# Performance work log

Measured on AMD Instinct MI355X. Metric: run time of the kernel, lower is better.

Reference implementation:

```python
import jax, jax.numpy as jnp
import numpy as np

T, BS, N, D_IN, D_OUT, H_FFN = 256, 64, 128, 64, 16, 64


def setup_inputs() -> dict:
    key = jax.random.key(0)
    ks = jax.random.split(key, 12)
    s = 1.0 / float(np.sqrt(D_IN))
    uni = lambda k, shp: jax.random.uniform(k, shp, jnp.float32, -s, s)
    return {
        "u": jax.random.normal(ks[0], (T, BS, D_IN), jnp.float32),
        "y": jax.random.normal(ks[1], (T, BS, D_OUT), jnp.float32),
        "W_ih": uni(ks[2], (D_IN, D_IN)),
        "W_hh": uni(ks[3], (D_IN, D_IN)),
        "b_ih": uni(ks[4], (D_IN,)),
        "b_hh": uni(ks[5], (D_IN,)),
        "W1": uni(ks[6], (D_IN, H_FFN)),
        "b1": uni(ks[7], (H_FFN,)),
        "W2": uni(ks[8], (H_FFN, D_OUT)),
        "b2": uni(ks[9], (D_OUT,)),
        # sigma matrices are diag(abs(rand(dim))) in torch; keep the diagonal vector
        "sigma_x_diag": jax.random.uniform(ks[10], (D_IN,), jnp.float32, 0.05, 1.0),
        "sigma_y_diag": jax.random.uniform(ks[11], (D_OUT,), jnp.float32, 0.05, 1.0),
    }


def reference(u, y, W_ih, W_hh, b_ih, b_hh, W1, b1, W2, b2, sigma_x_diag, sigma_y_diag):
    bs = u.shape[1]
    base = jax.random.key(42)
    # x0 = torch.randn(bs, N, input_size)
    x0 = jax.random.normal(jax.random.fold_in(base, 2**20), (bs, N, D_IN), jnp.float32)
    # MVN .sample() is detached from sigma params in torch
    std_x = jax.lax.stop_gradient(jnp.sqrt(sigma_x_diag))
    std_y = jax.lax.stop_gradient(jnp.sqrt(sigma_y_diag))
    sig_y = jax.lax.stop_gradient(sigma_y_diag)
    LOG2PI = jnp.log(jnp.asarray(2.0 * np.pi, jnp.float32))

    def ffn(x):
        return jax.nn.relu(x @ W1 + b1) @ W2 + b2

    def step(x, inp):
        u_k, y_k, t = inp
        k = jax.random.fold_in(base, t)
        k1, k2, k3 = jax.random.split(k, 3)
        # RNNCell(tanh); u_k broadcast over the particle dim (repeat_interleave in torch)
        x = jnp.tanh(u_k[:, None, :] @ W_ih + b_ih + x @ W_hh + b_hh)  # [bs,N,D_IN]
        x = x + std_x * jax.random.normal(k1, x.shape, x.dtype)        # eta noise
        x = jax.lax.stop_gradient(x)                                    # fisher: x.detach()
        y_hat = ffn(x) + std_y * jax.random.normal(k2, (bs, N, D_OUT), x.dtype)  # eps noise
        # log N(y_hat; y_k, diag(sigma_y)), fully detached (torch uses .detach())
        d = jax.lax.stop_gradient(y_hat) - y_k[:, None, :]
        logw = (-0.5 * jnp.sum(d * d / sig_y, axis=-1)
                - 0.5 * jnp.sum(jnp.log(sig_y)) - 0.5 * D_OUT * LOG2PI)  # [bs,N]
        # softmax + multinomial(w, N, replacement=True) == categorical on logits
        I = jax.random.categorical(k3, logw, axis=-1, shape=(N, bs)).T   # [bs,N]
        x = jnp.take_along_axis(x, I[:, :, None], axis=1)                # resample
        return x, y_hat

    ts = jnp.arange(u.shape[0], dtype=jnp.int32)
    _, preds = jax.lax.scan(step, x0, (u, y, ts))
    return preds  # [T, bs, N, D_OUT]
```

## Files before the change

### kernel.cpp

```cpp
#include <hip/hip_runtime.h>
#include <stdint.h>

#define TB 512

__device__ __forceinline__ uint32_t rotl32(uint32_t v, int s) {
    return (v << s) | (v >> (32 - s));
}

__device__ __forceinline__ void threefry2x32(uint32_t k0, uint32_t k1,
                                             uint32_t c0, uint32_t c1,
                                             uint32_t& o0, uint32_t& o1) {
    const uint32_t ks2 = k0 ^ k1 ^ 0x1BD11BDAu;
    uint32_t x0 = c0 + k0;
    uint32_t x1 = c1 + k1;
    x0 += x1; x1 = rotl32(x1, 13); x1 ^= x0;
    x0 += x1; x1 = rotl32(x1, 15); x1 ^= x0;
    x0 += x1; x1 = rotl32(x1, 26); x1 ^= x0;
    x0 += x1; x1 = rotl32(x1, 6);  x1 ^= x0;
    x0 += k1;  x1 += ks2 + 1u;
    x0 += x1; x1 = rotl32(x1, 17); x1 ^= x0;
    x0 += x1; x1 = rotl32(x1, 29); x1 ^= x0;
    x0 += x1; x1 = rotl32(x1, 16); x1 ^= x0;
    x0 += x1; x1 = rotl32(x1, 24); x1 ^= x0;
    x0 += ks2; x1 += k0 + 2u;
    x0 += x1; x1 = rotl32(x1, 13); x1 ^= x0;
    x0 += x1; x1 = rotl32(x1, 15); x1 ^= x0;
    x0 += x1; x1 = rotl32(x1, 26); x1 ^= x0;
    x0 += x1; x1 = rotl32(x1, 6);  x1 ^= x0;
    x0 += k0;  x1 += k1 + 3u;
    x0 += x1; x1 = rotl32(x1, 17); x1 ^= x0;
    x0 += x1; x1 = rotl32(x1, 29); x1 ^= x0;
    x0 += x1; x1 = rotl32(x1, 16); x1 ^= x0;
    x0 += x1; x1 = rotl32(x1, 24); x1 ^= x0;
    x0 += k1;  x1 += ks2 + 4u;
    x0 += x1; x1 = rotl32(x1, 13); x1 ^= x0;
    x0 += x1; x1 = rotl32(x1, 15); x1 ^= x0;
    x0 += x1; x1 = rotl32(x1, 26); x1 ^= x0;
    x0 += x1; x1 = rotl32(x1, 6);  x1 ^= x0;
    x0 += ks2; x1 += k0 + 5u;
    o0 = x0; o1 = x1;
}

__device__ __forceinline__ uint32_t jax_random_bits(uint32_t k0, uint32_t k1, uint32_t i) {
    uint32_t o0, o1;
    threefry2x32(k0, k1, 0u, i, o0, o1);
    return o0 ^ o1;
}

__device__ __forceinline__ float erfinv_f32(float x) {
    float w = -log1pf(-x * x);
    float p;
    if (w < 5.0f) {
        w = w - 2.5f;
        p = 2.81022636e-08f;
        p = fmaf(p, w, 3.43273939e-07f);
        p = fmaf(p, w, -3.5233877e-06f);
        p = fmaf(p, w, -4.39150654e-06f);
        p = fmaf(p, w, 0.00021858087f);
        p = fmaf(p, w, -0.00125372503f);
        p = fmaf(p, w, -0.00417768164f);
        p = fmaf(p, w, 0.246640727f);
        p = fmaf(p, w, 1.50140941f);
    } else {
        w = sqrtf(w) - 3.0f;
        p = -0.000200214257f;
        p = fmaf(p, w, 0.000100950558f);
        p = fmaf(p, w, 0.00134934322f);
        p = fmaf(p, w, -0.00367342844f);
        p = fmaf(p, w, 0.00573950773f);
        p = fmaf(p, w, -0.0076224613f);
        p = fmaf(p, w, 0.00943887047f);
        p = fmaf(p, w, 1.00167406f);
        p = fmaf(p, w, 2.83297682f);
    }
    return p * x;
}

__device__ __forceinline__ float normal_from_bits(uint32_t bits) {
    float f = __uint_as_float((bits >> 9) | 0x3F800000u) - 1.0f;
    float uu = fmaxf(-0.99999994f, fmaf(f, 2.0f, -0.99999994f));
    return 1.41421354f * erfinv_f32(uu);
}

__device__ __forceinline__ float gumbel_from_bits(uint32_t bits) {
    float f = __uint_as_float((bits >> 9) | 0x3F800000u) - 1.0f;
    float uu = fmaxf(1.17549435e-38f, f + 1.17549435e-38f);
    return -logf(-logf(uu));
}

__device__ __forceinline__ float jax_normal_elem(uint32_t k0, uint32_t k1, uint32_t i) {
    return normal_from_bits(jax_random_bits(k0, k1, i));
}

__device__ __forceinline__ void step_keys(int t, uint32_t& kx0, uint32_t& kx1,
                                          uint32_t& ky0, uint32_t& ky1,
                                          uint32_t& kc0, uint32_t& kc1) {
    uint32_t kk0, kk1;
    threefry2x32(0u, 42u, 0u, (uint32_t)t, kk0, kk1);
    threefry2x32(kk0, kk1, 0u, 0u, kx0, kx1);
    threefry2x32(kk0, kk1, 0u, 1u, ky0, ky1);
    threefry2x32(kk0, kk1, 0u, 2u, kc0, kc1);
}

constexpr size_t CONS_OFF  = 0;
constexpr size_t READY_OFF = 256;
constexpr size_t RING_OFF  = 65792;
constexpr int SLOT_FULL_F = 26688;
constexpr int SLOT_GUM_F  = 16384;
constexpr int XNZ_O = 0, ONZ_O = 8192, GUM_O = 10240, UBP_O = 26624;

__global__ __launch_bounds__(TB, 2) void smc_pc(
    const float* __restrict__ u, const float* __restrict__ y,
    const float* __restrict__ W_ih, const float* __restrict__ W_hh,
    const float* __restrict__ b_ih, const float* __restrict__ b_hh,
    const float* __restrict__ W1, const float* __restrict__ b1,
    const float* __restrict__ W2, const float* __restrict__ b2,
    const float* __restrict__ sigx, const float* __restrict__ sigy,
    float* __restrict__ out, float* __restrict__ ring,
    uint32_t* __restrict__ ready, uint32_t* __restrict__ cons,
    int R, int slotF, int mode) {
    const int bid = blockIdx.x;
    const int tid = threadIdx.x;
    const int b = bid & 63;

    if (bid >= 64) {
        const int k = (bid >> 6) - 1;
        for (int t = k; t < 256; t += 3) {
            if (t >= R) {
                if (tid == 0) {
                    while ((int)__hip_atomic_load(&cons[b], __ATOMIC_ACQUIRE,
                                                  __HIP_MEMORY_SCOPE_AGENT) < t - R + 1)
                        __builtin_amdgcn_s_sleep(8);
                }
                __syncthreads();
            }
            uint32_t kx0, kx1, ky0, ky1, kc0, kc1;
            step_keys(t, kx0, kx1, ky0, ky1, kc0, kc1);
            float* slot = ring + ((size_t)b * R + (size_t)(t % R)) * (size_t)slotF;
            if (mode == 0) {
                for (int it = tid; it < 8192; it += TB)
                    slot[XNZ_O + it] = jax_normal_elem(kx0, kx1, (uint32_t)(b * 8192 + it));
                for (int it = tid; it < 2048; it += TB)
                    slot[ONZ_O + it] = jax_normal_elem(ky0, ky1, (uint32_t)(b * 2048 + it));
                for (int it = tid; it < 16384; it += TB)
                    slot[GUM_O + it] = gumbel_from_bits(jax_random_bits(
                        kc0, kc1, ((uint32_t)(it >> 7) << 13) + (uint32_t)b * 128u + (uint32_t)(it & 127)));
                if (tid < 64) {
                    const float* ut = u + ((size_t)t * 64 + b) * 64;
                    float s = 0.f;
                    #pragma unroll 4
                    for (int k2 = 0; k2 < 64; ++k2) s = fmaf(ut[k2], W_ih[k2 * 64 + tid], s);
                    slot[UBP_O + tid] = s + b_ih[tid];
                }
            } else {
                for (int it = tid; it < 16384; it += TB)
                    slot[it] = gumbel_from_bits(jax_random_bits(
                        kc0, kc1, ((uint32_t)(it >> 7) << 13) + (uint32_t)b * 128u + (uint32_t)(it & 127)));
            }
            __threadfence();
            __syncthreads();
            if (tid == 0)
                __hip_atomic_store(&ready[b * 256 + t], 1u, __ATOMIC_RELEASE,
                                   __HIP_MEMORY_SCOPE_AGENT);
        }
        return;
    }

    __shared__ __align__(16) float xs[128][68];
    __shared__ __align__(16) float xn[128][68];
    __shared__ __align__(16) float Wihs[64][68];
    __shared__ __align__(16) float Whh[64][68];
    __shared__ __align__(16) float W1s[64][68];
    __shared__ __align__(16) float W2s[64][16];
    __shared__ __align__(16) float yh[128][16];
    __shared__ __align__(16) float logw[128];
    __shared__ __align__(16) float ubp[64];
    __shared__ float bhhs[64], b1s[64], b2s[16], stdxv[64], stdyv[16], sigyv[16], ykv[16];
    __shared__ int   anc[128];

    for (int i = tid; i < 4096; i += TB) {
        const int r = i >> 6, c = i & 63;
        Whh[r][c] = W_hh[i];
        W1s[r][c] = W1[i];
    }
    if (mode != 0)
        for (int i = tid; i < 4096; i += TB) Wihs[i >> 6][i & 63] = W_ih[i];
    for (int i = tid; i < 1024; i += TB) W2s[i >> 4][i & 15] = W2[i];
    if (tid < 64) { bhhs[tid] = b_hh[tid]; b1s[tid] = b1[tid]; stdxv[tid] = sqrtf(sigx[tid]); }
    if (tid < 16) { b2s[tid] = b2[tid]; sigyv[tid] = sigy[tid]; stdyv[tid] = sqrtf(sigy[tid]); }

    {
        uint32_t xk0, xk1;
        threefry2x32(0u, 42u, 0u, 1048576u, xk0, xk1);
        for (int it = tid; it < 8192; it += TB) {
            const uint32_t idx = (uint32_t)b * 8192u + (uint32_t)it;
            xs[it >> 6][it & 63] = jax_normal_elem(xk0, xk1, idx);
        }
    }
    __syncthreads();

    for (int t = 0; t < 256; ++t) {
        if (tid == 0) {
            if (!__hip_atomic_load(&ready[b * 256 + t], __ATOMIC_RELAXED,
                                   __HIP_MEMORY_SCOPE_AGENT)) {
                while (!__hip_atomic_load(&ready[b * 256 + t], __ATOMIC_RELAXED,
                                          __HIP_MEMORY_SCOPE_AGENT))
                    __builtin_amdgcn_s_sleep(2);
            }
            (void)__hip_atomic_load(&ready[b * 256 + t], __ATOMIC_ACQUIRE,
                                    __HIP_MEMORY_SCOPE_AGENT);
        }
        __syncthreads();
        const float* slot = ring + ((size_t)b * R + (size_t)(t % R)) * (size_t)slotF;
        const int gumOff = (mode == 0) ? GUM_O : 0;

        uint32_t kx0 = 0, kx1 = 0, ky0 = 0, ky1 = 0;
        if (mode != 0) {
            uint32_t kc0d, kc1d;
            step_keys(t, kx0, kx1, ky0, ky1, kc0d, kc1d);
        }

        const float* yt = y + ((size_t)t * 64 + b) * 16;
        if (mode == 0) {
            if (tid < 16) ((float4*)ubp)[tid] = ((const float4*)(slot + UBP_O))[tid];
            else if (tid < 32) ykv[tid - 16] = yt[tid - 16];
        } else {
            const float* ut = u + ((size_t)t * 64 + b) * 64;
            if (tid < 64) {
                float s = 0.f;
                #pragma unroll 4
                for (int k = 0; k < 64; ++k) s = fmaf(ut[k], Wihs[k][tid], s);
                ubp[tid] = s + b_ih[tid];
            }
            if (tid < 16) ykv[tid] = yt[tid];
        }
        __syncthreads();

        {
            const int n0 = (tid >> 4) * 4;
            const int d0 = (tid & 15) * 4;
            float acc[4][4];
            #pragma unroll
            for (int i = 0; i < 4; ++i)
                #pragma unroll
                for (int j = 0; j < 4; ++j) acc[i][j] = 0.f;
            #pragma unroll 4
            for (int k4 = 0; k4 < 64; k4 += 4) {
                float4 a[4];
                #pragma unroll
                for (int i = 0; i < 4; ++i) a[i] = *(const float4*)&xs[n0 + i][k4];
                #pragma unroll
                for (int kk = 0; kk < 4; ++kk) {
                    const float4 wr = *(const float4*)&Whh[k4 + kk][d0];
                    #pragma unroll
                    for (int i = 0; i < 4; ++i) {
                        const float av = (&a[i].x)[kk];
                        acc[i][0] = fmaf(av, wr.x, acc[i][0]);
                        acc[i][1] = fmaf(av, wr.y, acc[i][1]);
                        acc[i][2] = fmaf(av, wr.z, acc[i][2]);
                        acc[i][3] = fmaf(av, wr.w, acc[i][3]);
                    }
                }
            }
            #pragma unroll
            for (int i = 0; i < 4; ++i) {
                const int n = n0 + i;
                float4 res;
                #pragma unroll
                for (int j = 0; j < 4; ++j)
                    (&res.x)[j] = tanhf((ubp[d0 + j] + acc[i][j]) + bhhs[d0 + j]);
                *(float4*)&xn[n][d0] = res;
            }
            #pragma unroll
            for (int i = 0; i < 4; ++i) {
                const int n = n0 + i;
                float4 v = *(const float4*)&xn[n][d0];
                if (mode == 0) {
                    const float4 z = *(const float4*)&slot[XNZ_O + n * 64 + d0];
                    #pragma unroll
                    for (int j = 0; j < 4; ++j)
                        (&v.x)[j] = (&v.x)[j] + stdxv[d0 + j] * (&z.x)[j];
                } else {
                    #pragma unroll
                    for (int j = 0; j < 4; ++j) {
                        const int d = d0 + j;
                        const float nz = jax_normal_elem(kx0, kx1, (uint32_t)(b * 8192 + n * 64 + d));
                        (&v.x)[j] = (&v.x)[j] + stdxv[d] * nz;
                    }
                }
                *(float4*)&xn[n][d0] = v;
            }
        }
        __syncthreads();

        {
            const int n0 = (tid >> 4) * 4;
            const int d0 = (tid & 15) * 4;
            float acc[4][4];
            #pragma unroll
            for (int i = 0; i < 4; ++i)
                #pragma unroll
                for (int j = 0; j < 4; ++j) acc[i][j] = 0.f;
            #pragma unroll 4
            for (int k4 = 0; k4 < 64; k4 += 4) {
                float4 a[4];
                #pragma unroll
                for (int i = 0; i < 4; ++i) a[i] = *(const float4*)&xn[n0 + i][k4];
                #pragma unroll
                for (int kk = 0; kk < 4; ++kk) {
                    const float4 wr = *(const float4*)&W1s[k4 + kk][d0];
                    #pragma unroll
                    for (int i = 0; i < 4; ++i) {
                        const float av = (&a[i].x)[kk];
                        acc[i][0] = fmaf(av, wr.x, acc[i][0]);
                        acc[i][1] = fmaf(av, wr.y, acc[i][1]);
                        acc[i][2] = fmaf(av, wr.z, acc[i][2]);
                        acc[i][3] = fmaf(av, wr.w, acc[i][3]);
                    }
                }
            }
            #pragma unroll
            for (int i = 0; i < 4; ++i) {
                float4 res;
                #pragma unroll
                for (int j = 0; j < 4; ++j)
                    (&res.x)[j] = fmaxf(acc[i][j] + b1s[d0 + j], 0.0f);
                *(float4*)&xs[n0 + i][d0] = res;
            }
        }
        __syncthreads();

        {
            const int n = tid >> 2;
            const int d0 = (tid & 3) * 4;
            float4 acc = make_float4(0.f, 0.f, 0.f, 0.f);
            #pragma unroll 4
            for (int j4 = 0; j4 < 64; j4 += 4) {
                const float4 h4 = *(const float4*)&xs[n][j4];
                #pragma unroll
                for (int jj = 0; jj < 4; ++jj) {
                    const float4 wr = *(const float4*)&W2s[j4 + jj][d0];
                    const float hv = (&h4.x)[jj];
                    acc.x = fmaf(hv, wr.x, acc.x);
                    acc.y = fmaf(hv, wr.y, acc.y);
                    acc.z = fmaf(hv, wr.z, acc.z);
                    acc.w = fmaf(hv, wr.w, acc.w);
                }
            }
            float4 nz4;
            if (mode == 0) {
                nz4 = *(const float4*)&slot[ONZ_O + n * 16 + d0];
            } else {
                #pragma unroll
                for (int j = 0; j < 4; ++j)
                    (&nz4.x)[j] = jax_normal_elem(ky0, ky1, (uint32_t)(b * 2048 + n * 16 + d0 + j));
            }
            float4 res;
            #pragma unroll
            for (int j = 0; j < 4; ++j) {
                const int d = d0 + j;
                const float v = (&acc.x)[j] + b2s[d];
                const float yhv = v + stdyv[d] * (&nz4.x)[j];
                yh[n][d] = yhv;
                (&res.x)[j] = yhv;
            }
            *(float4*)&out[(((size_t)t * 64 + b) * 128 + n) * 16 + d0] = res;
        }
        __syncthreads();

        if (tid < 128) {
            float s = 0.f;
            for (int d = 0; d < 16; ++d) {
                const float dd = yh[tid][d] - ykv[d];
                s += (dd * dd) / sigyv[d];
            }
            logw[tid] = -0.5f * s;
        }
        __syncthreads();

        {
            const int p = tid >> 2;
            const int sub = tid & 3;
            const float* gp = slot + gumOff + p * 128 + (sub << 5);
            float best = -3.402823466e+38f;
            int bi = 0;
            for (int m4 = 0; m4 < 32; m4 += 4) {
                const float4 g4 = *(const float4*)&gp[m4];
                #pragma unroll
                for (int j = 0; j < 4; ++j) {
                    const int n = (sub << 5) + m4 + j;
                    const float v = logw[n] + (&g4.x)[j];
                    if (v > best) { best = v; bi = n; }
                }
            }
            #pragma unroll
            for (int off = 1; off < 4; off <<= 1) {
                const float ov = __shfl_xor(best, off);
                const int   oi = __shfl_xor(bi, off);
                if (ov > best || (ov == best && oi < bi)) { best = ov; bi = oi; }
            }
            if (sub == 0) anc[p] = bi;
        }
        __syncthreads();

        for (int it = tid; it < 2048; it += TB) {
            const int n = it >> 4, qq = (it & 15) * 4;
            *(float4*)&xs[n][qq] = *(const float4*)&xn[anc[n]][qq];
        }
        __syncthreads();

        if (tid == 0)
            __hip_atomic_store(&cons[b], (uint32_t)(t + 1), __ATOMIC_RELEASE,
                               __HIP_MEMORY_SCOPE_AGENT);
    }
}

__global__ __launch_bounds__(TB, 2) void smc_mono(
    const float* __restrict__ u, const float* __restrict__ y,
    const float* __restrict__ W_ih, const float* __restrict__ W_hh,
    const float* __restrict__ b_ih, const float* __restrict__ b_hh,
    const float* __restrict__ W1, const float* __restrict__ b1,
    const float* __restrict__ W2, const float* __restrict__ b2,
    const float* __restrict__ sigx, const float* __restrict__ sigy,
    float* __restrict__ out) {
    const int b = blockIdx.x;
    const int tid = threadIdx.x;

    __shared__ __align__(16) float xs[128][68];
    __shared__ __align__(16) float xn[128][68];
    __shared__ __align__(16) float Wihs[64][68];
    __shared__ __align__(16) float Whh[64][68];
    __shared__ __align__(16) float W1s[64][68];
    __shared__ __align__(16) float W2s[64][16];
    __shared__ __align__(16) float yh[128][16];
    __shared__ float logw[128];
    __shared__ float ubp[64];
    __shared__ float bhhs[64], b1s[64], b2s[16], stdxv[64], stdyv[16], sigyv[16], ykv[16];
    __shared__ int   anc[128];

    for (int i = tid; i < 4096; i += TB) {
        const int r = i >> 6, c = i & 63;
        Wihs[r][c] = W_ih[i];
        Whh[r][c]  = W_hh[i];
        W1s[r][c]  = W1[i];
    }
    for (int i = tid; i < 1024; i += TB) W2s[i >> 4][i & 15] = W2[i];
    if (tid < 64) { bhhs[tid] = b_hh[tid]; b1s[tid] = b1[tid]; stdxv[tid] = sqrtf(sigx[tid]); }
    if (tid < 16) { b2s[tid] = b2[tid]; sigyv[tid] = sigy[tid]; stdyv[tid] = sqrtf(sigy[tid]); }

    {
        uint32_t xk0, xk1;
        threefry2x32(0u, 42u, 0u, 1048576u, xk0, xk1);
        for (int it = tid; it < 8192; it += TB) {
            const uint32_t idx = (uint32_t)b * 8192u + (uint32_t)it;
            xs[it >> 6][it & 63] = jax_normal_elem(xk0, xk1, idx);
        }
    }
    __syncthreads();

    for (int t = 0; t < 256; ++t) {
        uint32_t kx0, kx1, ky0, ky1, kc0, kc1;
        step_keys(t, kx0, kx1, ky0, ky1, kc0, kc1);

        const float* ut = u + ((size_t)t * 64 + b) * 64;
        const float* yt = y + ((size_t)t * 64 + b) * 16;
        if (tid < 64) {
            float s = 0.f;
            #pragma unroll 4
            for (int k = 0; k < 64; ++k) s = fmaf(ut[k], Wihs[k][tid], s);
            ubp[tid] = s + b_ih[tid];
        }
        if (tid < 16) ykv[tid] = yt[tid];
        __syncthreads();

        {
            const int n0 = (tid >> 4) * 4;
            const int d0 = (tid & 15) * 4;
            float acc[4][4];
            #pragma unroll
            for (int i = 0; i < 4; ++i)
                #pragma unroll
                for (int j = 0; j < 4; ++j) acc[i][j] = 0.f;
            #pragma unroll 4
            for (int k4 = 0; k4 < 64; k4 += 4) {
                float4 a[4];
                #pragma unroll
                for (int i = 0; i < 4; ++i) a[i] = *(const float4*)&xs[n0 + i][k4];
                #pragma unroll
                for (int kk = 0; kk < 4; ++kk) {
                    const float4 wr = *(const float4*)&Whh[k4 + kk][d0];
                    #pragma unroll
                    for (int i = 0; i < 4; ++i) {
                        const float av = (&a[i].x)[kk];
                        acc[i][0] = fmaf(av, wr.x, acc[i][0]);
                        acc[i][1] = fmaf(av, wr.y, acc[i][1]);
                        acc[i][2] = fmaf(av, wr.z, acc[i][2]);
                        acc[i][3] = fmaf(av, wr.w, acc[i][3]);
                    }
                }
            }
            #pragma unroll
            for (int i = 0; i < 4; ++i) {
                const int n = n0 + i;
                float4 res;
                #pragma unroll
                for (int j = 0; j < 4; ++j) {
                    const int d = d0 + j;
                    (&res.x)[j] = tanhf((ubp[d] + acc[i][j]) + bhhs[d]);
                }
                *(float4*)&xn[n][d0] = res;
            }
            #pragma unroll
            for (int i = 0; i < 4; ++i) {
                const int n = n0 + i;
                float4 v = *(const float4*)&xn[n][d0];
                #pragma unroll
                for (int j = 0; j < 4; ++j) {
                    const int d = d0 + j;
                    const uint32_t idx = (uint32_t)(b * 8192 + n * 64 + d);
                    (&v.x)[j] = (&v.x)[j] + stdxv[d] * jax_normal_elem(kx0, kx1, idx);
                }
                *(float4*)&xn[n][d0] = v;
            }
        }
        __syncthreads();

        {
            const int n0 = (tid >> 4) * 4;
            const int d0 = (tid & 15) * 4;
            float acc[4][4];
            #pragma unroll
            for (int i = 0; i < 4; ++i)
                #pragma unroll
                for (int j = 0; j < 4; ++j) acc[i][j] = 0.f;
            #pragma unroll 4
            for (int k4 = 0; k4 < 64; k4 += 4) {
                float4 a[4];
                #pragma unroll
                for (int i = 0; i < 4; ++i) a[i] = *(const float4*)&xn[n0 + i][k4];
                #pragma unroll
                for (int kk = 0; kk < 4; ++kk) {
                    const float4 wr = *(const float4*)&W1s[k4 + kk][d0];
                    #pragma unroll
                    for (int i = 0; i < 4; ++i) {
                        const float av = (&a[i].x)[kk];
                        acc[i][0] = fmaf(av, wr.x, acc[i][0]);
                        acc[i][1] = fmaf(av, wr.y, acc[i][1]);
                        acc[i][2] = fmaf(av, wr.z, acc[i][2]);
                        acc[i][3] = fmaf(av, wr.w, acc[i][3]);
                    }
                }
            }
            #pragma unroll
            for (int i = 0; i < 4; ++i) {
                float4 res;
                #pragma unroll
                for (int j = 0; j < 4; ++j)
                    (&res.x)[j] = fmaxf(acc[i][j] + b1s[d0 + j], 0.0f);
                *(float4*)&xs[n0 + i][d0] = res;
            }
        }
        __syncthreads();

        {
            const int n = tid >> 2;
            const int d0 = (tid & 3) * 4;
            float4 acc = make_float4(0.f, 0.f, 0.f, 0.f);
            #pragma unroll 4
            for (int j4 = 0; j4 < 64; j4 += 4) {
                const float4 h4 = *(const float4*)&xs[n][j4];
                #pragma unroll
                for (int jj = 0; jj < 4; ++jj) {
                    const float4 wr = *(const float4*)&W2s[j4 + jj][d0];
                    const float hv = (&h4.x)[jj];
                    acc.x = fmaf(hv, wr.x, acc.x);
                    acc.y = fmaf(hv, wr.y, acc.y);
                    acc.z = fmaf(hv, wr.z, acc.z);
                    acc.w = fmaf(hv, wr.w, acc.w);
                }
            }
            float4 res;
            #pragma unroll
            for (int j = 0; j < 4; ++j) {
                const int d = d0 + j;
                const float v = (&acc.x)[j] + b2s[d];
                const float nz = jax_normal_elem(ky0, ky1, (uint32_t)(b * 2048 + n * 16 + d));
                const float yhv = v + stdyv[d] * nz;
                yh[n][d] = yhv;
                (&res.x)[j] = yhv;
            }
            *(float4*)&out[(((size_t)t * 64 + b) * 128 + n) * 16 + d0] = res;
        }
        __syncthreads();

        if (tid < 128) {
            float s = 0.f;
            for (int d = 0; d < 16; ++d) {
                const float dd = yh[tid][d] - ykv[d];
                s += (dd * dd) / sigyv[d];
            }
            logw[tid] = -0.5f * s;
        }
        __syncthreads();

        {
            const int p = tid >> 2;
            const int sub = tid & 3;
            float best = -3.402823466e+38f;
            int bi = 0;
            const uint32_t base_idx = (uint32_t)p * 8192u + (uint32_t)b * 128u;
            for (int m = 0; m < 32; ++m) {
                const int n = (sub << 5) + m;
                const float v = logw[n] + gumbel_from_bits(jax_random_bits(kc0, kc1, base_idx + (uint32_t)n));
                if (v > best) { best = v; bi = n; }
            }
            #pragma unroll
            for (int off = 1; off < 4; off <<= 1) {
                const float ov = __shfl_xor(best, off);
                const int   oi = __shfl_xor(bi, off);
                if (ov > best || (ov == best && oi < bi)) { best = ov; bi = oi; }
            }
            if (sub == 0) anc[p] = bi;
        }
        __syncthreads();

        for (int it = tid; it < 2048; it += TB) {
            const int n = it >> 4, qq = (it & 15) * 4;
            *(float4*)&xs[n][qq] = *(const float4*)&xn[anc[n]][qq];
        }
        __syncthreads();
    }
}

extern "C" void kernel_launch(void* const* d_in, const int* in_sizes, int n_in,
                              void* d_out, int out_size, void* d_ws, size_t ws_size,
                              hipStream_t stream) {
    const float* u    = (const float*)d_in[0];
    const float* y    = (const float*)d_in[1];
    const float* W_ih = (const float*)d_in[2];
    const float* W_hh = (const float*)d_in[3];
    const float* b_ih = (const float*)d_in[4];
    const float* b_hh = (const float*)d_in[5];
    const float* W1   = (const float*)d_in[6];
    const float* b1   = (const float*)d_in[7];
    const float* W2   = (const float*)d_in[8];
    const float* b2   = (const float*)d_in[9];
    const float* sigx = (const float*)d_in[10];
    const float* sigy = (const float*)d_in[11];
    float* out = (float*)d_out;

    const size_t needF3 = RING_OFF + (size_t)64 * 3 * SLOT_FULL_F * 4;
    const size_t needF2 = RING_OFF + (size_t)64 * 2 * SLOT_FULL_F * 4;
    const size_t needG2 = RING_OFF + (size_t)64 * 2 * SLOT_GUM_F * 4;
    int mode = -1, R = 0, slotF = 0;
    if (ws_size >= needF3)      { mode = 0; R = 3; slotF = SLOT_FULL_F; }
    else if (ws_size >= needF2) { mode = 0; R = 2; slotF = SLOT_FULL_F; }
    else if (ws_size >= needG2) { mode = 1; R = 2; slotF = SLOT_GUM_F; }

    if (mode >= 0) {
        uint32_t* cons  = (uint32_t*)((char*)d_ws + CONS_OFF);
        uint32_t* ready = (uint32_t*)((char*)d_ws + READY_OFF);
        float*    ring  = (float*)((char*)d_ws + RING_OFF);
        hipMemsetAsync(d_ws, 0, RING_OFF, stream);
        void* args[] = {
            (void*)&u, (void*)&y, (void*)&W_ih, (void*)&W_hh, (void*)&b_ih,
            (void*)&b_hh, (void*)&W1, (void*)&b1, (void*)&W2, (void*)&b2,
            (void*)&sigx, (void*)&sigy, (void*)&out, (void*)&ring,
            (void*)&ready, (void*)&cons, (void*)&R, (void*)&slotF, (void*)&mode};
        hipLaunchCooperativeKernel((const void*)smc_pc, dim3(256), dim3(TB),
                                   args, 0, stream);
    } else {
        hipLaunchKernelGGL(smc_mono, dim3(64), dim3(TB), 0, stream,
                           u, y, W_ih, W_hh, b_ih, b_hh, W1, b1, W2, b2, sigx, sigy, out);
    }
}
```

Before: 9.730 ms.

## Double threads per block in producer-consumer SMC kernel and restructure per-thread work

Raises the block size of the cooperative producer/consumer kernel from 512 to 1024 threads. Each thread now computes 2x4 instead of 4x4 outputs in the RNN and FFN matmuls, and W2 is stored transposed so each thread computes 2 outputs. Other changes fuse tanh with the noise add, read the ubp projection straight from the ring slot, and prefetch the Gumbel values early so the resampling argmax uses 8 lanes per particle. The goal is to shorten the serial per-step critical path with more parallelism, at the cost of higher register pressure and possible co-residency limits for the cooperative launch.

```diff
diff --git a/kernel.cpp b/kernel.cpp
--- a/kernel.cpp
+++ b/kernel.cpp
@@ -1,7 +1,8 @@
 #include <hip/hip_runtime.h>
 #include <stdint.h>
 
-#define TB 512
+#define TB 1024
+#define TBM 512
 
 __device__ __forceinline__ uint32_t rotl32(uint32_t v, int s) {
     return (v << s) | (v >> (32 - s));
@@ -109,7 +110,7 @@
 constexpr int SLOT_GUM_F  = 16384;
 constexpr int XNZ_O = 0, ONZ_O = 8192, GUM_O = 10240, UBP_O = 26624;
 
-__global__ __launch_bounds__(TB, 2) void smc_pc(
+__global__ __launch_bounds__(TB, 4) void smc_pc(
     const float* __restrict__ u, const float* __restrict__ y,
     const float* __restrict__ W_ih, const float* __restrict__ W_hh,
     const float* __restrict__ b_ih, const float* __restrict__ b_hh,
@@ -171,10 +172,10 @@
     __shared__ __align__(16) float Wihs[64][68];
     __shared__ __align__(16) float Whh[64][68];
     __shared__ __align__(16) float W1s[64][68];
-    __shared__ __align__(16) float W2s[64][16];
+    __shared__ __align__(16) float W2t[16][68];
     __shared__ __align__(16) float yh[128][16];
-    __shared__ __align__(16) float logw[128];
-    __shared__ __align__(16) float ubp[64];
+    __shared__ float logw[128];
+    __shared__ float ubp[64];
     __shared__ float bhhs[64], b1s[64], b2s[16], stdxv[64], stdyv[16], sigyv[16], ykv[16];
     __shared__ int   anc[128];
 
@@ -185,7 +186,7 @@
     }
     if (mode != 0)
         for (int i = tid; i < 4096; i += TB) Wihs[i >> 6][i & 63] = W_ih[i];
-    for (int i = tid; i < 1024; i += TB) W2s[i >> 4][i & 15] = W2[i];
+    for (int i = tid; i < 1024; i += TB) W2t[i & 15][i >> 4] = W2[i];
     if (tid < 64) { bhhs[tid] = b_hh[tid]; b1s[tid] = b1[tid]; stdxv[tid] = sqrtf(sigx[tid]); }
     if (tid < 16) { b2s[tid] = b2[tid]; sigyv[tid] = sigy[tid]; stdyv[tid] = sqrtf(sigy[tid]); }
 
@@ -219,12 +220,9 @@
             uint32_t kc0d, kc1d;
             step_keys(t, kx0, kx1, ky0, ky1, kc0d, kc1d);
         }
-
         const float* yt = y + ((size_t)t * 64 + b) * 16;
-        if (mode == 0) {
-            if (tid < 16) ((float4*)ubp)[tid] = ((const float4*)(slot + UBP_O))[tid];
-            else if (tid < 32) ykv[tid - 16] = yt[tid - 16];
-        } else {
+
+        if (mode != 0) {
             const float* ut = u + ((size_t)t * 64 + b) * 64;
             if (tid < 64) {
                 float s = 0.f;
@@ -232,95 +230,84 @@
                 for (int k = 0; k < 64; ++k) s = fmaf(ut[k], Wihs[k][tid], s);
                 ubp[tid] = s + b_ih[tid];
             }
+            __syncthreads();
+        }
+
+        {
             if (tid < 16) ykv[tid] = yt[tid];
-        }
-        __syncthreads();
-
-        {
-            const int n0 = (tid >> 4) * 4;
+            const int n0 = (tid >> 4) * 2;
             const int d0 = (tid & 15) * 4;
-            float acc[4][4];
-            #pragma unroll
-            for (int i = 0; i < 4; ++i)
-                #pragma unroll
-                for (int j = 0; j < 4; ++j) acc[i][j] = 0.f;
+            float4 ub4;
+            if (mode == 0) ub4 = *(const float4*)(slot + UBP_O + d0);
+            else           ub4 = *(const float4*)&ubp[d0];
+            float acc[2][4] = {{0.f,0.f,0.f,0.f},{0.f,0.f,0.f,0.f}};
             #pragma unroll 4
             for (int k4 = 0; k4 < 64; k4 += 4) {
-                float4 a[4];
-                #pragma unroll
-                for (int i = 0; i < 4; ++i) a[i] = *(const float4*)&xs[n0 + i][k4];
+                const float4 a0 = *(const float4*)&xs[n0][k4];
+                const float4 a1 = *(const float4*)&xs[n0 + 1][k4];
                 #pragma unroll
                 for (int kk = 0; kk < 4; ++kk) {
                     const float4 wr = *(const float4*)&Whh[k4 + kk][d0];
-                    #pragma unroll
-                    for (int i = 0; i < 4; ++i) {
-                        const float av = (&a[i].x)[kk];
-                        acc[i][0] = fmaf(av, wr.x, acc[i][0]);
-                        acc[i][1] = fmaf(av, wr.y, acc[i][1]);
-                        acc[i][2] = fmaf(av, wr.z, acc[i][2]);
-                        acc[i][3] = fmaf(av, wr.w, acc[i][3]);
-                    }
-                }
-            }
-            #pragma unroll
-            for (int i = 0; i < 4; ++i) {
+                    const float av0 = (&a0.x)[kk], av1 = (&a1.x)[kk];
+                    acc[0][0] = fmaf(av0, wr.x, acc[0][0]);
+                    acc[0][1] = fmaf(av0, wr.y, acc[0][1]);
+                    acc[0][2] = fmaf(av0, wr.z, acc[0][2]);
+                    acc[0][3] = fmaf(av0, wr.w, acc[0][3]);
+                    acc[1][0] = fmaf(av1, wr.x, acc[1][0]);
+                    acc[1][1] = fmaf(av1, wr.y, acc[1][1]);
+                    acc[1][2] = fmaf(av1, wr.z, acc[1][2]);
+                    acc[1][3] = fmaf(av1, wr.w, acc[1][3]);
+                }
+            }
+            #pragma unroll
+            for (int i = 0; i < 2; ++i) {
                 const int n = n0 + i;
                 float4 res;
-                #pragma unroll
-                for (int j = 0; j < 4; ++j)
-                    (&res.x)[j] = tanhf((ubp[d0 + j] + acc[i][j]) + bhhs[d0 + j]);
-                *(float4*)&xn[n][d0] = res;
-            }
-            #pragma unroll
-            for (int i = 0; i < 4; ++i) {
-                const int n = n0 + i;
-                float4 v = *(const float4*)&xn[n][d0];
                 if (mode == 0) {
                     const float4 z = *(const float4*)&slot[XNZ_O + n * 64 + d0];
                     #pragma unroll
-                    for (int j = 0; j < 4; ++j)
-                        (&v.x)[j] = (&v.x)[j] + stdxv[d0 + j] * (&z.x)[j];
+                    for (int j = 0; j < 4; ++j) {
+                        const float v = tanhf(((&ub4.x)[j] + acc[i][j]) + bhhs[d0 + j]);
+                        (&res.x)[j] = v + stdxv[d0 + j] * (&z.x)[j];
+                    }
                 } else {
                     #pragma unroll
                     for (int j = 0; j < 4; ++j) {
                         const int d = d0 + j;
+                        const float v = tanhf(((&ub4.x)[j] + acc[i][j]) + bhhs[d]);
                         const float nz = jax_normal_elem(kx0, kx1, (uint32_t)(b * 8192 + n * 64 + d));
-                        (&v.x)[j] = (&v.x)[j] + stdxv[d] * nz;
+                        (&res.x)[j] = v + stdxv[d] * nz;
                     }
                 }
-                *(float4*)&xn[n][d0] = v;
-            }
-        }
-        __syncthreads();
-
-        {
-            const int n0 = (tid >> 4) * 4;
+                *(float4*)&xn[n][d0] = res;
+            }
+        }
+        __syncthreads();
+
+        {
+            const int n0 = (tid >> 4) * 2;
             const int d0 = (tid & 15) * 4;
-            float acc[4][4];
-            #pragma unroll
-            for (int i = 0; i < 4; ++i)
-                #pragma unroll
-                for (int j = 0; j < 4; ++j) acc[i][j] = 0.f;
+            float acc[2][4] = {{0.f,0.f,0.f,0.f},{0.f,0.f,0.f,0.f}};
             #pragma unroll 4
             for (int k4 = 0; k4 < 64; k4 += 4) {
-                float4 a[4];
-                #pragma unroll
-                for (int i = 0; i < 4; ++i) a[i] = *(const float4*)&xn[n0 + i][k4];
+                const float4 a0 = *(const float4*)&xn[n0][k4];
+                const float4 a1 = *(const float4*)&xn[n0 + 1][k4];
                 #pragma unroll
                 for (int kk = 0; kk < 4; ++kk) {
                     const float4 wr = *(const float4*)&W1s[k4 + kk][d0];
-                    #pragma unroll
-                    for (int i = 0; i < 4; ++i) {
-                        const float av = (&a[i].x)[kk];
-                        acc[i][0] = fmaf(av, wr.x, acc[i][0]);
-                        acc[i][1] = fmaf(av, wr.y, acc[i][1]);
-                        acc[i][2] = fmaf(av, wr.z, acc[i][2]);
-                        acc[i][3] = fmaf(av, wr.w, acc[i][3]);
-                    }
-                }
-            }
-            #pragma unroll
-            for (int i = 0; i < 4; ++i) {
+                    const float av0 = (&a0.x)[kk], av1 = (&a1.x)[kk];
+                    acc[0][0] = fmaf(av0, wr.x, acc[0][0]);
+                    acc[0][1] = fmaf(av0, wr.y, acc[0][1]);
+                    acc[0][2] = fmaf(av0, wr.z, acc[0][2]);
+                    acc[0][3] = fmaf(av0, wr.w, acc[0][3]);
+                    acc[1][0] = fmaf(av1, wr.x, acc[1][0]);
+                    acc[1][1] = fmaf(av1, wr.y, acc[1][1]);
+                    acc[1][2] = fmaf(av1, wr.z, acc[1][2]);
+                    acc[1][3] = fmaf(av1, wr.w, acc[1][3]);
+                }
+            }
+            #pragma unroll
+            for (int i = 0; i < 2; ++i) {
                 float4 res;
                 #pragma unroll
                 for (int j = 0; j < 4; ++j)
@@ -330,41 +317,45 @@
         }
         __syncthreads();
 
-        {
-            const int n = tid >> 2;
-            const int d0 = (tid & 3) * 4;
-            float4 acc = make_float4(0.f, 0.f, 0.f, 0.f);
+        float4 g0, g1, g2, g3;
+        {
+            const int n = tid >> 3;
+            const int sub = tid & 7;
+            const float* gpre = slot + gumOff + n * 128 + (sub << 4);
+            g0 = ((const float4*)gpre)[0];
+            g1 = ((const float4*)gpre)[1];
+            g2 = ((const float4*)gpre)[2];
+            g3 = ((const float4*)gpre)[3];
+
+            const int d0 = sub * 2;
+            float accx = 0.f, accy = 0.f;
             #pragma unroll 4
             for (int j4 = 0; j4 < 64; j4 += 4) {
                 const float4 h4 = *(const float4*)&xs[n][j4];
-                #pragma unroll
-                for (int jj = 0; jj < 4; ++jj) {
-                    const float4 wr = *(const float4*)&W2s[j4 + jj][d0];
-                    const float hv = (&h4.x)[jj];
-                    acc.x = fmaf(hv, wr.x, acc.x);
-                    acc.y = fmaf(hv, wr.y, acc.y);
-                    acc.z = fmaf(hv, wr.z, acc.z);
-                    acc.w = fmaf(hv, wr.w, acc.w);
-                }
-            }
-            float4 nz4;
+                const float4 wa = *(const float4*)&W2t[d0][j4];
+                const float4 wb = *(const float4*)&W2t[d0 + 1][j4];
+                accx = fmaf(h4.x, wa.x, accx);
+                accx = fmaf(h4.y, wa.y, accx);
+                accx = fmaf(h4.z, wa.z, accx);
+                accx = fmaf(h4.w, wa.w, accx);
+                accy = fmaf(h4.x, wb.x, accy);
+                accy = fmaf(h4.y, wb.y, accy);
+                accy = fmaf(h4.z, wb.z, accy);
+                accy = fmaf(h4.w, wb.w, accy);
+            }
+            float2 z2;
             if (mode == 0) {
-                nz4 = *(const float4*)&slot[ONZ_O + n * 16 + d0];
+                z2 = *(const float2*)&slot[ONZ_O + n * 16 + d0];
             } else {
-                #pragma unroll
-                for (int j = 0; j < 4; ++j)
-                    (&nz4.x)[j] = jax_normal_elem(ky0, ky1, (uint32_t)(b * 2048 + n * 16 + d0 + j));
-            }
-            float4 res;
-            #pragma unroll
-            for (int j = 0; j < 4; ++j) {
-                const int d = d0 + j;
-                const float v = (&acc.x)[j] + b2s[d];
-                const float yhv = v + stdyv[d] * (&nz4.x)[j];
-                yh[n][d] = yhv;
-                (&res.x)[j] = yhv;
-            }
-            *(float4*)&out[(((size_t)t * 64 + b) * 128 + n) * 16 + d0] = res;
+                z2.x = jax_normal_elem(ky0, ky1, (uint32_t)(b * 2048 + n * 16 + d0));
+                z2.y = jax_normal_elem(ky0, ky1, (uint32_t)(b * 2048 + n * 16 + d0 + 1));
+            }
+            float2 res;
+            res.x = (accx + b2s[d0])     + stdyv[d0]     * z2.x;
+            res.y = (accy + b2s[d0 + 1]) + stdyv[d0 + 1] * z2.y;
+            yh[n][d0]     = res.x;
+            yh[n][d0 + 1] = res.y;
+            *(float2*)&out[(((size_t)t * 64 + b) * 128 + n) * 16 + d0] = res;
         }
         __syncthreads();
 
@@ -379,22 +370,23 @@
         __syncthreads();
 
         {
-            const int p = tid >> 2;
-            const int sub = tid & 3;
-            const float* gp = slot + gumOff + p * 128 + (sub << 5);
+            const int p = tid >> 3;
+            const int sub = tid & 7;
+            const int nb = sub << 4;
             float best = -3.402823466e+38f;
             int bi = 0;
-            for (int m4 = 0; m4 < 32; m4 += 4) {
-                const float4 g4 = *(const float4*)&gp[m4];
+            const float4 gs[4] = {g0, g1, g2, g3};
+            #pragma unroll
+            for (int q4 = 0; q4 < 4; ++q4) {
                 #pragma unroll
                 for (int j = 0; j < 4; ++j) {
-                    const int n = (sub << 5) + m4 + j;
-                    const float v = logw[n] + (&g4.x)[j];
+                    const int n = nb + q4 * 4 + j;
+                    const float v = logw[n] + (&gs[q4].x)[j];
                     if (v > best) { best = v; bi = n; }
                 }
             }
             #pragma unroll
-            for (int off = 1; off < 4; off <<= 1) {
+            for (int off = 1; off < 8; off <<= 1) {
                 const float ov = __shfl_xor(best, off);
                 const int   oi = __shfl_xor(bi, off);
                 if (ov > best || (ov == best && oi < bi)) { best = ov; bi = oi; }
@@ -415,7 +407,7 @@
     }
 }
 
-__global__ __launch_bounds__(TB, 2) void smc_mono(
+__global__ __launch_bounds__(TBM, 2) void smc_mono(
     const float* __restrict__ u, const float* __restrict__ y,
     const float* __restrict__ W_ih, const float* __restrict__ W_hh,
     const float* __restrict__ b_ih, const float* __restrict__ b_hh,
@@ -438,20 +430,20 @@
     __shared__ float bhhs[64], b1s[64], b2s[16], stdxv[64], stdyv[16], sigyv[16], ykv[16];
     __shared__ int   anc[128];
 
-    for (int i = tid; i < 4096; i += TB) {
+    for (int i = tid; i < 4096; i += TBM) {
         const int r = i >> 6, c = i & 63;
         Wihs[r][c] = W_ih[i];
         Whh[r][c]  = W_hh[i];
         W1s[r][c]  = W1[i];
     }
-    for (int i = tid; i < 1024; i += TB) W2s[i >> 4][i & 15] = W2[i];
+    for (int i = tid; i < 1024; i += TBM) W2s[i >> 4][i & 15] = W2[i];
     if (tid < 64) { bhhs[tid] = b_hh[tid]; b1s[tid] = b1[tid]; stdxv[tid] = sqrtf(sigx[tid]); }
     if (tid < 16) { b2s[tid] = b2[tid]; sigyv[tid] = sigy[tid]; stdyv[tid] = sqrtf(sigy[tid]); }
 
     {
         uint32_t xk0, xk1;
         threefry2x32(0u, 42u, 0u, 1048576u, xk0, xk1);
-        for (int it = tid; it < 8192; it += TB) {
+        for (int it = tid; it < 8192; it += TBM) {
             const uint32_t idx = (uint32_t)b * 8192u + (uint32_t)it;
             xs[it >> 6][it & 63] = jax_normal_elem(xk0, xk1, idx);
         }
@@ -624,7 +616,7 @@
         }
         __syncthreads();
 
-        for (int it = tid; it < 2048; it += TB) {
+        for (int it = tid; it < 2048; it += TBM) {
             const int n = it >> 4, qq = (it & 15) * 4;
             *(float4*)&xs[n][qq] = *(const float4*)&xn[anc[n]][qq];
         }
@@ -670,7 +662,7 @@
         hipLaunchCooperativeKernel((const void*)smc_pc, dim3(256), dim3(TB),
                                    args, 0, stream);
     } else {
-        hipLaunchKernelGGL(smc_mono, dim3(64), dim3(TB), 0, stream,
+        hipLaunchKernelGGL(smc_mono, dim3(64), dim3(TBM), 0, stream,
                            u, y, W_ih, W_hh, b_ih, b_hh, W1, b1, W2, b2, sigx, sigy, out);
     }
 }
```

New measurement: 10.40 ms. +6.9%, slower.
